# Optimization experiments

Hardware: AMD Instinct MI355X
Metric: run time of the kernel (lower is better)

Reference implementation:

```python
import jax, jax.numpy as jnp
import numpy as np

DN = ('NCHW', 'OIHW', 'NCHW')
B, T, D, H, W = 8, 10, 10, 128, 128
WINDOW_OUT = 5


def conv2d(x, w, b):
    y = jax.lax.conv_general_dilated(x, w, (1, 1), 'SAME', dimension_numbers=DN)
    return y + b[None, :, None, None]


def lstm_cell(x, h, c, w, b):
    # ConvLSTM gate update: conv over [x; h], split into i,f,o,g
    z = conv2d(jnp.concatenate([x, h], axis=1), w, b)
    i, f, o, g = jnp.split(z, 4, axis=1)
    c2 = jax.nn.sigmoid(f) * c + jax.nn.sigmoid(i) * jnp.tanh(g)
    h2 = jax.nn.sigmoid(o) * jnp.tanh(c2)
    return h2, c2


def attn_score(x, h, c, w1, b1, w2, b2):
    # conv-MLP attention score over concat([x, h, c]) -> (b, H, W)
    z = jnp.concatenate([x, h, c], axis=1)
    return conv2d(jnp.tanh(conv2d(z, w1, b1)), w2, b2)[:, 0]


def setup_inputs():
    key = jax.random.key(0)
    ks = jax.random.split(key, 16)
    s = 0.05
    return {
        'x': jax.random.normal(ks[0], (B, T, D, H, W), jnp.float32),
        'h0': jnp.zeros((B, 1, H, W), jnp.float32),
        'c0': jnp.zeros((B, 1, H, W), jnp.float32),
        'h1': jnp.zeros((B, 64, H, W), jnp.float32),
        'c1': jnp.zeros((B, 64, H, W), jnp.float32),
        # encoder cells: layer0 (in 10, hid 1), layer1 (in 1, hid 64)
        'w_enc0': jax.random.normal(ks[1], (4, 11, 3, 3), jnp.float32) * s,
        'b_enc0': jax.random.normal(ks[2], (4,), jnp.float32) * s,
        'w_enc1': jax.random.normal(ks[3], (256, 65, 3, 3), jnp.float32) * s,
        'b_enc1': jax.random.normal(ks[4], (256,), jnp.float32) * s,
        # decoder cells: layer0 (in 1, hid 64), layer1 (in 64, hid 1)
        'w_dec0': jax.random.normal(ks[5], (256, 65, 3, 3), jnp.float32) * s,
        'b_dec0': jax.random.normal(ks[6], (256,), jnp.float32) * s,
        'w_dec1': jax.random.normal(ks[7], (4, 65, 3, 3), jnp.float32) * s,
        'b_dec1': jax.random.normal(ks[8], (4,), jnp.float32) * s,
        # input attention: in 10+2*1=12 -> 32 -> 1
        'wa1': jax.random.normal(ks[9], (32, 12, 3, 3), jnp.float32) * s,
        'ba1': jax.random.normal(ks[10], (32,), jnp.float32) * s,
        'wa2': jax.random.normal(ks[11], (1, 32, 3, 3), jnp.float32) * s,
        'ba2': jax.random.normal(ks[12], (1,), jnp.float32) * s,
        # temporal attention: in 1+2*64=129 -> 32 -> 1
        'wt1': jax.random.normal(ks[13], (32, 129, 3, 3), jnp.float32) * s,
        'bt1': jax.random.normal(ks[14], (32,), jnp.float32) * s,
        'wt2': jax.random.normal(ks[15], (1, 32, 3, 3), jnp.float32) * s,
        'bt2': jnp.zeros((1,), jnp.float32),
    }


def reference(x, h0, c0, h1, c1, w_enc0, b_enc0, w_enc1, b_enc1,
              w_dec0, b_dec0, w_dec1, b_dec1,
              wa1, ba1, wa2, ba2, wt1, bt1, wt2, bt2):
    def input_attn(xx, h, c):
        # per-feature score; vmap over feature dim k (axis 2 of x)
        score = jax.vmap(lambda xk: attn_score(xk, h, c, wa1, ba1, wa2, ba2),
                         in_axes=2, out_axes=1)(xx)          # (b, D, H, W)
        alpha = jax.nn.softmax(score, axis=1)
        return xx * alpha[:, None]                            # broadcast over time

    # ---- encoder layer 0: input attention re-weights x every step (compounding)
    def step0(carry, t):
        xx, h, c = carry
        xx = input_attn(xx, h, c)
        h, c = lstm_cell(xx[:, t], h, c, w_enc0, b_enc0)
        return (xx, h, c), (h, c)

    _, (hs0, cs0) = jax.lax.scan(step0, (x, h0, c0), jnp.arange(T))
    hs0 = jnp.moveaxis(hs0, 0, 1)   # (b, T, 1, H, W)
    cs0 = jnp.moveaxis(cs0, 0, 1)

    # ---- encoder layer 1
    def step1(carry, xt):
        h, c = lstm_cell(xt, carry[0], carry[1], w_enc1, b_enc1)
        return (h, c), (h, c)

    _, (hs1, cs1) = jax.lax.scan(step1, (h1, c1), jnp.moveaxis(hs0, 1, 0))
    hs1 = jnp.moveaxis(hs1, 0, 1)   # (b, T, 64, H, W)
    cs1 = jnp.moveaxis(cs1, 0, 1)

    def temporal_attn(y, hb, cb):
        score = jax.vmap(lambda ht, ct: attn_score(y, ht, ct, wt1, bt1, wt2, bt2),
                         in_axes=1, out_axes=1)(hb, cb)       # (b, T, H, W)
        beta = jax.nn.softmax(score, axis=1)
        return jnp.sum(hb * beta[:, :, None], axis=1), cb[:, -1]

    # ---- decoder: states reversed -> layer0 uses encoder layer1 states, etc.
    y0 = x[:, -1, 0][:, None]       # x[:, [-1], selected_dim] -> (b, 1, H, W)

    def dec_step(carry, _):
        y, hb0, cb0, hb1, cb1 = carry
        ht, ct = temporal_attn(y, hb0, cb0)
        ht, ct = lstm_cell(y, ht, ct, w_dec0, b_dec0)
        y = ht
        hb0 = jnp.concatenate([hb0[:, 1:], ht[:, None]], axis=1)
        cb0 = jnp.concatenate([cb0[:, 1:], ct[:, None]], axis=1)
        ht2, ct2 = lstm_cell(y, hb1[:, -1], cb1[:, -1], w_dec1, b_dec1)
        y = ht2
        hb1 = jnp.concatenate([hb1[:, 1:], ht2[:, None]], axis=1)
        cb1 = jnp.concatenate([cb1[:, 1:], ct2[:, None]], axis=1)
        return (y, hb0, cb0, hb1, cb1), y

    _, ys = jax.lax.scan(dec_step, (y0, hs1, cs1, hs0, cs0), None, length=WINDOW_OUT)
    return jnp.moveaxis(ys, 0, 1)   # (b, window_out, 1, H, W)
```

## Files before the change

kernel.cpp:

```cpp
#include <hip/hip_runtime.h>


#define PX 16384L
#define T_ 10
#define D_ 10

__device__ __forceinline__ float fast_tanh(float x) {
    const float e = __builtin_exp2f(x * 2.88539008f);
    return 1.f - 2.f * __builtin_amdgcn_rcpf(e + 1.f);
}
__device__ __forceinline__ float fast_sig(float x) {
    const float e = __builtin_exp2f(x * -1.44269504f);
    return __builtin_amdgcn_rcpf(e + 1.f);
}
__device__ __forceinline__ float fast_exp(float x) {
    return __builtin_exp2f(x * 1.44269504f);
}

__device__ __forceinline__ void lstm_dev(
    float* lds,
    int tile, int hcb, int b,
    const float* __restrict__ in0, long bs0,
    const float* __restrict__ in1,
    const float* __restrict__ w, const float* __restrict__ bias,
// ... 63 lines not shown
    for (int j = 0; j < 2; j++) {
        const int hc = hc0 + j;
        const float bi = bias[hc], bf = bias[64 + hc];
        const float bo = bias[128 + hc], bg = bias[192 + hc];
#pragma unroll
        for (int rr = 0; rr < 2; rr++) {
            const long opix = (long)(tileY + r0 + rr) * 128 + tileX + tx;
            const float i_ = fast_sig(acc[(j * 4 + 0) * 2 + rr] + bi);
            const float f_ = fast_sig(acc[(j * 4 + 1) * 2 + rr] + bf);
            const float o_ = fast_sig(acc[(j * 4 + 2) * 2 + rr] + bo);
            const float g_ = fast_tanh(acc[(j * 4 + 3) * 2 + rr] + bg);
            const float cp = cprev[((long)b * 64 + hc) * PX + opix];
            const float c2 = f_ * cp + i_ * g_;
            const float h2 = o_ * fast_tanh(c2);
            hout[((long)b * 64 + hc) * PX + opix] = h2;
            cout_[((long)b * 64 + hc) * PX + opix] = c2;
        }
    }
}

__device__ __forceinline__ void zpart_dev(
    float* lds,
    int tile, int cob, int b,
    const float* __restrict__ hsrc, const float* __restrict__ csrc,
    const float* __restrict__ wt1, const float* __restrict__ bt1,
    float* __restrict__ zdst)
{
    const int tid = threadIdx.x;
    const int tx = tid & 15, ty = tid >> 4;
    const int tileX = (tile & 7) << 4, tileY = (tile >> 3) << 4;
    const int co0 = cob << 3;
    float acc[8];
#pragma unroll
    for (int j = 0; j < 8; j++) acc[j] = 0.f;

    int g0[2]; float m0[2];
#pragma unroll
    for (int i = 0; i < 2; i++) {
        const int lidx = tid + i * 256;
        const int r = lidx / 18, cc = lidx - r * 18;
        const int gy = tileY + r - 1, gx = tileX + cc - 1;
        const bool inb = (lidx < 324) && ((unsigned)gy < 128u) && ((unsigned)gx < 128u);
        g0[i] = inb ? gy * 128 + gx : 0;
        m0[i] = inb ? 1.f : 0.f;
    }

    for (int cb = 0; cb < 128; cb += 4) {
        for (int cl = 0; cl < 4; cl++) {
            const int ci = cb + cl;
            const float* p = (ci < 64) ? hsrc + ((long)b * 64 + ci) * PX
                                       : csrc + ((long)b * 64 + (ci - 64)) * PX;
#pragma unroll
            for (int i = 0; i < 2; i++) {
                const int lidx = tid + i * 256;
                if (lidx < 324) lds[cl * 324 + lidx] = m0[i] * p[g0[i]];
            }
        }
        __syncthreads();
        for (int cl = 0; cl < 4; cl++) {
            float r9[9];
#pragma unroll
            for (int dy = 0; dy < 3; dy++)
#pragma unroll
                for (int dx = 0; dx < 3; dx++)
                    r9[dy * 3 + dx] = lds[cl * 324 + (ty + dy) * 18 + tx + dx];
            const int ci = cb + cl;
#pragma unroll
            for (int j = 0; j < 8; j++) {
                const float* wp = wt1 + ((long)(co0 + j) * 129 + 1 + ci) * 9;
                float a = acc[j];
#pragma unroll
                for (int q = 0; q < 9; q++) a = fmaf(wp[q], r9[q], a);
                acc[j] = a;
            }
        }
        __syncthreads();
    }
    const long opix = (long)(tileY + ty) * 128 + tileX + tx;
#pragma unroll
    for (int j = 0; j < 8; j++)
        zdst[((long)b * 32 + co0 + j) * PX + opix] = acc[j] + bt1[co0 + j];
}

__global__ __launch_bounds__(256)
void lstm_merge_k(const float* __restrict__ in0, long bs0,
                  const float* __restrict__ in1,
                  const float* __restrict__ w, const float* __restrict__ bias,
                  const float* __restrict__ cprev,
                  float* __restrict__ hout, float* __restrict__ cout_,
                  const float* __restrict__ zh, const float* __restrict__ zc,
                  float* __restrict__ zdst,
                  const float* __restrict__ wt1, const float* __restrict__ bt1)
{
    __shared__ float lds[8 * 612];
    const int bid = blockIdx.x, b = blockIdx.z;
    if (bid < 1024) {
        lstm_dev(lds, bid & 31, bid >> 5, b, in0, bs0, in1, w, bias,
                 cprev, hout, cout_);
    } else {
        const int q = bid - 1024;
        zpart_dev(lds, q & 63, q >> 6, b, zh, zc, wt1, bt1, zdst);
    }
}

__global__ __launch_bounds__(256)
void zpart_k(const float* __restrict__ zh, const float* __restrict__ zc,
             float* __restrict__ zdst,
             const float* __restrict__ wt1, const float* __restrict__ bt1)
{
    __shared__ float lds[4 * 324];
    zpart_dev(lds, blockIdx.x, blockIdx.y, blockIdx.z, zh, zc, wt1, bt1, zdst);
}

__global__ __launch_bounds__(256)
void dec_merge_k(const float* __restrict__ hs1s,
                 const float* __restrict__ hb1, long hb1bs,
                 const float* __restrict__ w1,
                 float* __restrict__ l1p, int nbs,
                 const float* __restrict__ zc, float* __restrict__ zdst,
                 const float* __restrict__ wt1, const float* __restrict__ bt1)
{
    __shared__ float lds[4 * 324];
    const int bid = blockIdx.x, b = blockIdx.z;
    if (bid < 256) {
        const int tile = bid & 63, s = bid >> 6;
        const int ci0 = (s == 0) ? 0 : (s == 1) ? 17 : (s == 2) ? 33 : 49;
        const int cn  = (s == 0) ? 17 : 16;
        const int tid = threadIdx.x;
        const int tx = tid & 15, ty = tid >> 4;
        const int tileX = (tile & 7) << 4, tileY = (tile >> 3) << 4;
        int g0[2]; float m0[2];
#pragma unroll
        for (int i = 0; i < 2; i++) {
            const int lidx = tid + i * 256;
            const int r = lidx / 18, cc = lidx - r * 18;
            const int gy = tileY + r - 1, gx = tileX + cc - 1;
            const bool inb = (lidx < 324) && ((unsigned)gy < 128u) && ((unsigned)gx < 128u);
            g0[i] = inb ? gy * 128 + gx : 0;
            m0[i] = inb ? 1.f : 0.f;
        }
        float acc[4] = {0.f, 0.f, 0.f, 0.f};
        for (int cb = 0; cb < cn; cb += 4) {
            const int cmax = min(4, cn - cb);
            for (int cl = 0; cl < cmax; cl++) {
                const int ci = ci0 + cb + cl;
                const float* p = (ci < 64) ? hs1s + ((long)b * 64 + ci) * PX
                                           : hb1 + (long)b * hb1bs;
#pragma unroll
                for (int i = 0; i < 2; i++) {
                    const int lidx = tid + i * 256;
                    if (lidx < 324) lds[cl * 324 + lidx] = m0[i] * p[g0[i]];
                }
            }
            __syncthreads();
            for (int cl = 0; cl < cmax; cl++) {
                float r9[9];
#pragma unroll
                for (int dy = 0; dy < 3; dy++)
#pragma unroll
                    for (int dx = 0; dx < 3; dx++)
                        r9[dy * 3 + dx] = lds[cl * 324 + (ty + dy) * 18 + tx + dx];
                const int ci = ci0 + cb + cl;
#pragma unroll
                for (int j = 0; j < 4; j++) {
                    const float* wp = w1 + ((long)j * 65 + ci) * 9;
                    float a = acc[j];
#pragma unroll
                    for (int q = 0; q < 9; q++) a = fmaf(wp[q], r9[q], a);
                    acc[j] = a;
                }
            }
            __syncthreads();
        }
        const long opix = (long)(tileY + ty) * 128 + tileX + tx;
#pragma unroll
        for (int j = 0; j < 4; j++)
            l1p[(((long)s * nbs + b) * 4 + j) * PX + opix] = acc[j];
    } else {
        const int q = bid - 256;
        zpart_dev(lds, q & 63, q >> 6, b, hs1s, zc, wt1, bt1, zdst);
    }
}

__global__ __launch_bounds__(256)
void combine_lstm_k(const float* __restrict__ pbuf, int nsl, int hidden,
                    const float* __restrict__ bias,
                    const float* __restrict__ cprev, long cpbs,
                    float* __restrict__ hout, long hobs,
                    float* __restrict__ cout_, long cobs,
                    float* __restrict__ hout2, long ho2bs, int rb, int nbs)
{
    const long idx = (long)blockIdx.x * 256 + threadIdx.x;
    if (idx >= (long)rb * hidden * PX) return;
    const long px = idx & 16383;
    const long v = idx >> 14;
    const int hc = (int)(v % hidden), b = (int)(v / hidden);
    const int nco = 4 * hidden;
    float g4[4] = {0.f, 0.f, 0.f, 0.f};
    for (int s = 0; s < nsl; s++)
#pragma unroll
        for (int g = 0; g < 4; g++)
            g4[g] += pbuf[(((long)s * nbs + b) * nco + g * hidden + hc) * PX + px];
    const float i_ = fast_sig(g4[0] + bias[hc]);
    const float f_ = fast_sig(g4[1] + bias[hidden + hc]);
    const float o_ = fast_sig(g4[2] + bias[2 * hidden + hc]);
    const float g_ = fast_tanh(g4[3] + bias[3 * hidden + hc]);
    const float cp = cprev[(long)b * cpbs + (long)hc * PX + px];
    const float c2 = f_ * cp + i_ * g_;
    const float h2 = o_ * fast_tanh(c2);
    hout[(long)b * hobs + (long)hc * PX + px] = h2;
    cout_[(long)b * cobs + (long)hc * PX + px] = c2;
    if (hout2) hout2[(long)b * ho2bs + (long)hc * PX + px] = h2;
}

__global__ __launch_bounds__(256)
void enc0_lstm_k(const float* __restrict__ x, int t, const float* __restrict__ A,
                 const float* __restrict__ hprev, const float* __restrict__ cprev,
                 const float* __restrict__ w, const float* __restrict__ bias,
                 float* __restrict__ hout, float* __restrict__ cout_)
{
    __shared__ float lds[4 * 324];
    const int tid = threadIdx.x;
    const int tx = tid & 15, ty = tid >> 4;
    const int tile = blockIdx.x, b = blockIdx.z;
    const int tileX = (tile & 7) << 4, tileY = (tile >> 3) << 4;
    int g0[2]; float m0[2];
#pragma unroll
    for (int i = 0; i < 2; i++) {
        const int lidx = tid + i * 256;
        const int r = lidx / 18, cc = lidx - r * 18;
        const int gy = tileY + r - 1, gx = tileX + cc - 1;
        const bool inb = (lidx < 324) && ((unsigned)gy < 128u) && ((unsigned)gx < 128u);
        g0[i] = inb ? gy * 128 + gx : 0;
        m0[i] = inb ? 1.f : 0.f;
    }
    float acc[4] = {0.f, 0.f, 0.f, 0.f};
    for (int cb = 0; cb < 11; cb += 4) {
        const int cmax = min(4, 11 - cb);
        for (int cl = 0; cl < cmax; cl++) {
            const int ci = cb + cl;
#pragma unroll
            for (int i = 0; i < 2; i++) {
                const int lidx = tid + i * 256;
                if (lidx < 324) {
                    float v;
                    if (ci < 10) {
                        v = x[(((long)b * T_ + t) * D_ + ci) * PX + g0[i]]
                            * A[((long)b * 10 + ci) * PX + g0[i]];
                    } else {
                        v = hprev[(long)b * PX + g0[i]];
                    }
                    lds[cl * 324 + lidx] = m0[i] * v;
                }
            }
        }
        __syncthreads();
        for (int cl = 0; cl < cmax; cl++) {
            float r9[9];
#pragma unroll
            for (int dy = 0; dy < 3; dy++)
#pragma unroll
                for (int dx = 0; dx < 3; dx++)
                    r9[dy * 3 + dx] = lds[cl * 324 + (ty + dy) * 18 + tx + dx];
            const int ci = cb + cl;
#pragma unroll
            for (int g = 0; g < 4; g++) {
                const float* wp = w + ((long)g * 11 + ci) * 9;
                float a = acc[g];
#pragma unroll
                for (int q = 0; q < 9; q++) a = fmaf(wp[q], r9[q], a);
                acc[g] = a;
            }
        }
        __syncthreads();
    }
    const long opix = (long)(tileY + ty) * 128 + tileX + tx;
    const float i_ = fast_sig(acc[0] + bias[0]);
    const float f_ = fast_sig(acc[1] + bias[1]);
    const float o_ = fast_sig(acc[2] + bias[2]);
    const float g_ = fast_tanh(acc[3] + bias[3]);
    const float cp = cprev[(long)b * PX + opix];
    const float c2 = f_ * cp + i_ * g_;
    const float h2 = o_ * fast_tanh(c2);
    hout[(long)b * PX + opix] = h2;
    cout_[(long)b * PX + opix] = c2;
}

__global__ __launch_bounds__(256)
void iattn_k(const float* __restrict__ x, const float* __restrict__ A,
             const float* __restrict__ h, const float* __restrict__ c,
             const float* __restrict__ wa1, const float* __restrict__ ba1,
             const float* __restrict__ wa2, const float* __restrict__ ba2,
             float* __restrict__ score)
{
    __shared__ float xl[12][400];
    __shared__ float zl[8][324];
    const int tid = threadIdx.x;
    const int tileX = (blockIdx.x & 7) << 4, tileY = (blockIdx.x >> 3) << 4;
    const int z = blockIdx.z;
    const int b = z & 7, k = z >> 3;

    int g0[2]; float m0[2]; float aTr[2];
#pragma unroll
    for (int i = 0; i < 2; i++) {
        const int lidx = tid + i * 256;
        const int r = lidx / 20, cc = lidx - r * 20;
        const int gy = tileY + r - 2, gx = tileX + cc - 2;
        const bool inb = (lidx < 400) && ((unsigned)gy < 128u) && ((unsigned)gx < 128u);
        g0[i] = inb ? gy * 128 + gx : 0;
        m0[i] = inb ? 1.f : 0.f;
        aTr[i] = A ? (m0[i] * A[((long)b * 10 + k) * PX + g0[i]]) : 1.f;
    }
    for (int ch = 0; ch < 12; ch++) {
        const float* p = (ch < 10) ? x + (((long)b * 10 + ch) * 10 + k) * PX
                       : (ch == 10) ? h + (long)b * PX : c + (long)b * PX;
#pragma unroll
        for (int i = 0; i < 2; i++) {
            const int lidx = tid + i * 256;
            if (lidx < 400) {
                float v = m0[i] * p[g0[i]];
                if (ch < 10) v *= aTr[i];
                xl[ch][lidx] = v;
            }
        }
    }
    __syncthreads();

    const int i0 = tid;
    const int i1 = tid + 256;
    const int zr0 = i0 / 18, zc0 = i0 - zr0 * 18;
    const int zr1 = (i1 < 324) ? i1 / 18 : 0;
    const int zc1 = (i1 < 324) ? i1 - zr1 * 18 : 0;
    const int gy0 = tileY + zr0 - 1, gx0 = tileX + zc0 - 1;
    const bool in0_ = ((unsigned)gy0 < 128u) && ((unsigned)gx0 < 128u);
    const int gy1 = tileY + zr1 - 1, gx1 = tileX + zc1 - 1;
    const bool in1_ = (i1 < 324) && ((unsigned)gy1 < 128u) && ((unsigned)gx1 < 128u);

    const int tx = tid & 15, ty = tid >> 4;
    float sacc = ba2[0];

    for (int hf = 0; hf < 4; hf++) {
        float acc0[8], acc1[8];
#pragma unroll
        for (int co = 0; co < 8; co++) { acc0[co] = 0.f; acc1[co] = 0.f; }
        for (int ci = 0; ci < 12; ci++) {
            float wA[9], wB[9];
#pragma unroll
            for (int dy = 0; dy < 3; dy++)
#pragma unroll
                for (int dx = 0; dx < 3; dx++) {
                    wA[dy * 3 + dx] = xl[ci][(zr0 + dy) * 20 + zc0 + dx];
                    wB[dy * 3 + dx] = xl[ci][(zr1 + dy) * 20 + zc1 + dx];
                }
#pragma unroll
            for (int co = 0; co < 8; co++) {
                const float* wp = wa1 + ((long)(hf * 8 + co) * 12 + ci) * 9;
                float a0 = acc0[co], a1 = acc1[co];
#pragma unroll
                for (int q = 0; q < 9; q++) {
                    a0 = fmaf(wp[q], wA[q], a0);
                    a1 = fmaf(wp[q], wB[q], a1);
                }
                acc0[co] = a0; acc1[co] = a1;
            }
        }
        if (hf) __syncthreads();
#pragma unroll
        for (int co = 0; co < 8; co++) {
            zl[co][i0] = in0_ ? fast_tanh(acc0[co] + ba1[hf * 8 + co]) : 0.f;
            if (i1 < 324) zl[co][i1] = in1_ ? fast_tanh(acc1[co] + ba1[hf * 8 + co]) : 0.f;
        }
        __syncthreads();
        for (int co = 0; co < 8; co++) {
            const float* wp = wa2 + (hf * 8 + co) * 9;
#pragma unroll
            for (int ky = 0; ky < 3; ky++)
#pragma unroll
                for (int kx = 0; kx < 3; kx++)
                    sacc = fmaf(wp[ky * 3 + kx], zl[co][(ty + ky) * 18 + tx + kx], sacc);
        }
    }
    score[((long)b * 10 + k) * PX + (long)(tileY + ty) * 128 + tileX + tx] = sacc;
}

__global__ __launch_bounds__(256)
void softmax_mul_k(const float* __restrict__ s, float* __restrict__ A, int nb, int init)
{
    const long idx = (long)blockIdx.x * 256 + threadIdx.x;
    if (idx >= (long)nb * PX) return;
    const long b = idx >> 14, p = idx & 16383;
    const float* base = s + b * 10 * PX + p;
    float v[10]; float m = -1e30f;
#pragma unroll
    for (int t = 0; t < 10; t++) { v[t] = base[t * PX]; m = fmaxf(m, v[t]); }
    float sum = 0.f;
#pragma unroll
    for (int t = 0; t < 10; t++) { v[t] = fast_exp(v[t] - m); sum += v[t]; }
    const float r = __builtin_amdgcn_rcpf(sum);
    float* Ab = A + b * 10 * PX + p;
#pragma unroll
    for (int t = 0; t < 10; t++)
        Ab[t * PX] = init ? (v[t] * r) : (Ab[t * PX] * v[t] * r);
}

__global__ __launch_bounds__(256)
void attn_fuse_k(const float* __restrict__ y, long ybs,
                 const float* __restrict__ zpart,
                 const float* __restrict__ wt1,
                 const float* __restrict__ wt2, const float* __restrict__ bt2,
                 float* __restrict__ score, int rb, int nbs)
{
    __shared__ float ylds[400];
    __shared__ float zl[16][324];
    const int tid = threadIdx.x;
    const int tileX = (blockIdx.x & 7) << 4, tileY = (blockIdx.x >> 3) << 4;
    const int z = blockIdx.z;
    const int b = z % rb, t = z / rb;

#pragma unroll
    for (int i = 0; i < 2; i++) {
        const int lidx = tid + i * 256;
        if (lidx < 400) {
            const int r = lidx / 20, cc = lidx - r * 20;
            const int gy = tileY + r - 2, gx = tileX + cc - 2;
            const bool inb = ((unsigned)gy < 128u) && ((unsigned)gx < 128u);
            ylds[lidx] = inb ? y[(long)b * ybs + gy * 128 + gx] : 0.f;
        }
    }
    __syncthreads();

    const int i0 = tid, i1 = tid + 256;
    const int zr0 = i0 / 18, zc0 = i0 - zr0 * 18;
    const int zr1 = (i1 < 324) ? i1 / 18 : 0;
    const int zc1 = (i1 < 324) ? i1 - zr1 * 18 : 0;
    const int gy0 = tileY + zr0 - 1, gx0 = tileX + zc0 - 1;
    const bool in0_ = ((unsigned)gy0 < 128u) && ((unsigned)gx0 < 128u);
    const int gy1 = tileY + zr1 - 1, gx1 = tileX + zc1 - 1;
    const bool in1_ = (i1 < 324) && ((unsigned)gy1 < 128u) && ((unsigned)gx1 < 128u);
    const long pix0 = in0_ ? (long)gy0 * 128 + gx0 : 0;
    const long pix1 = in1_ ? (long)gy1 * 128 + gx1 : 0;
    const float* zp0 = zpart + ((long)t * nbs + b) * 32 * PX;

    const int tx = tid & 15, ty = tid >> 4;
    float sacc = bt2[0];

    for (int hf = 0; hf < 2; hf++) {
        float yw0[9], yw1[9];
#pragma unroll
        for (int dy = 0; dy < 3; dy++)
#pragma unroll
            for (int dx = 0; dx < 3; dx++) {
                yw0[dy * 3 + dx] = ylds[(zr0 + dy) * 20 + zc0 + dx];
                yw1[dy * 3 + dx] = ylds[(zr1 + dy) * 20 + zc1 + dx];
            }
        if (hf) __syncthreads();
#pragma unroll 4
        for (int ch = 0; ch < 16; ch++) {
            const int cg = hf * 16 + ch;
            const float* wy = wt1 + (long)cg * 129 * 9;
            float s0 = zp0[(long)cg * PX + pix0];
            float s1 = (i1 < 324) ? zp0[(long)cg * PX + pix1] : 0.f;
#pragma unroll
            for (int q = 0; q < 9; q++) {
                s0 = fmaf(wy[q], yw0[q], s0);
                s1 = fmaf(wy[q], yw1[q], s1);
            }
            zl[ch][i0] = in0_ ? fast_tanh(s0) : 0.f;
            if (i1 < 324) zl[ch][i1] = in1_ ? fast_tanh(s1) : 0.f;
        }
        __syncthreads();
        for (int ch = 0; ch < 16; ch++) {
            const float* wp = wt2 + (hf * 16 + ch) * 9;
#pragma unroll
            for (int ky = 0; ky < 3; ky++)
#pragma unroll
                for (int kx = 0; kx < 3; kx++)
                    sacc = fmaf(wp[ky * 3 + kx], zl[ch][(ty + ky) * 18 + tx + kx], sacc);
        }
    }
    score[((long)b * 10 + t) * PX + (long)(tileY + ty) * 128 + tileX + tx] = sacc;
}

__global__ __launch_bounds__(256)
void smax_wsum_k(const float* __restrict__ score, const float* __restrict__ hs1,
                 float* __restrict__ aht, int rb, int nbs)
{
    const long idx = (long)blockIdx.x * 256 + threadIdx.x;
    if (idx >= (long)rb * PX) return;
    const long b = idx >> 14, p = idx & 16383;
    const int ch0 = blockIdx.y * 8;
    const float* base = score + b * 10 * PX + p;
    float v[10]; float m = -1e30f;
#pragma unroll
    for (int t = 0; t < 10; t++) { v[t] = base[t * PX]; m = fmaxf(m, v[t]); }
    float sum = 0.f;
#pragma unroll
    for (int t = 0; t < 10; t++) { v[t] = fast_exp(v[t] - m); sum += v[t]; }
    const float r = __builtin_amdgcn_rcpf(sum);
#pragma unroll
    for (int t = 0; t < 10; t++) v[t] *= r;
    const long slot1 = (long)nbs * 64 * PX;
#pragma unroll
    for (int j = 0; j < 8; j++) {
        const int ch = ch0 + j;
        float a = 0.f;
#pragma unroll
        for (int t = 0; t < 10; t++)
            a += v[t] * hs1[t * slot1 + (b * 64 + ch) * PX + p];
        aht[(b * 64 + ch) * PX + p] = a;
    }
}

extern "C" void kernel_launch(void* const* d_in, const int* in_sizes, int n_in,
                              void* d_out, int out_size, void* d_ws, size_t ws_size,
                              hipStream_t stream)
{
    const float* x      = (const float*)d_in[0];
    const float* h0     = (const float*)d_in[1];
    const float* c0in   = (const float*)d_in[2];
    const float* h1     = (const float*)d_in[3];
    const float* c1     = (const float*)d_in[4];
    const float* w_enc0 = (const float*)d_in[5];
    const float* b_enc0 = (const float*)d_in[6];
    const float* w_enc1 = (const float*)d_in[7];
    const float* b_enc1 = (const float*)d_in[8];
    const float* w_dec0 = (const float*)d_in[9];
    const float* b_dec0 = (const float*)d_in[10];
    const float* w_dec1 = (const float*)d_in[11];
    const float* b_dec1 = (const float*)d_in[12];
    const float* wa1 = (const float*)d_in[13];
    const float* ba1 = (const float*)d_in[14];
    const float* wa2 = (const float*)d_in[15];
    const float* ba2 = (const float*)d_in[16];
    const float* wt1 = (const float*)d_in[17];
    const float* bt1 = (const float*)d_in[18];
    const float* wt2 = (const float*)d_in[19];
    const float* bt2 = (const float*)d_in[20];
    float* out = (float*)d_out;

    const int tiers[7] = {8, 6, 5, 4, 3, 2, 1};
    int nb = 0;
    for (int ti = 0; ti < 7; ti++) {
        const size_t need = (size_t)(160 + 1188 * tiers[ti]) * PX * sizeof(float);
        if (need <= ws_size) { nb = tiers[ti]; break; }
    }
    if (nb == 0) return;

    float* ws = (float*)d_ws;
    float* hs0 = ws;
    float* cs0 = hs0 + 80 * PX;
    float* G   = cs0 + 80 * PX;
    float* A    = G;
    float* sc1  = G + 80 * PX;
    const long slot1  = (long)nb * 64 * PX;
    float* hs1   = G;
    float* cs1   = hs1 + 10 * slot1;
    float* zpart = cs1 + 2 * slot1;
    float* aht   = zpart + (long)10 * nb * 32 * PX;
    float* l1p   = aht + (long)nb * 64 * PX;
    float* hs0g  = l1p + (long)4 * nb * 4 * PX;
    float* cs0g  = hs0g + (long)5 * nb * PX;
    float* scD   = cs0g + (long)5 * nb * PX;

    const dim3 blk(256);
    const long TDP = (long)T_ * D_ * PX;
    const long zslot = (long)nb * 32 * PX;

    for (int t = 0; t < 10; t++) {
        const float* hprev = (t == 0) ? h0 : hs0 + (long)(t - 1) * 8 * PX;
        const float* cprev = (t == 0) ? c0in : cs0 + (long)(t - 1) * 8 * PX;
        iattn_k<<<dim3(64, 1, 80), blk, 0, stream>>>(
            x, (t == 0) ? nullptr : A, hprev, cprev, wa1, ba1, wa2, ba2, sc1);
        softmax_mul_k<<<512, blk, 0, stream>>>(sc1, A, 8, t == 0);
        enc0_lstm_k<<<dim3(64, 1, 8), blk, 0, stream>>>(
            x, t, A, hprev, cprev, w_enc0, b_enc0,
            hs0 + (long)t * 8 * PX, cs0 + (long)t * 8 * PX);
    }

    for (int b0 = 0; b0 < 8; b0 += nb) {
        const int rb = (8 - b0 < nb) ? (8 - b0) : nb;
        const float* xb  = x + (long)b0 * TDP;
        float* outb = out + (long)b0 * 5 * PX;

        for (int t = 0; t < 10; t++) {
            const float* hprev = (t == 0) ? h1 + (long)b0 * 64 * PX
                                          : hs1 + (long)(t - 1) * slot1;
            const float* cprev = (t == 0) ? c1 + (long)b0 * 64 * PX
                                          : cs1 + (long)((t - 1) & 1) * slot1;
            const int gx = (t == 0) ? 1024 : 1280;
            lstm_merge_k<<<dim3(gx, 1, rb), blk, 0, stream>>>(
                hs0 + (long)t * 8 * PX + (long)b0 * PX, PX,
                hprev, w_enc1, b_enc1, cprev,
                hs1 + (long)t * slot1, cs1 + (long)(t & 1) * slot1,
                (t == 0) ? nullptr : hs1 + (long)(t - 1) * slot1,
                (t == 0) ? nullptr : cs1 + (long)((t - 1) & 1) * slot1,
                (t == 0) ? nullptr : zpart + (long)(t - 1) * zslot,
                wt1, bt1);
        }
        zpart_k<<<dim3(64, 4, rb), blk, 0, stream>>>(
            hs1 + 9L * slot1, cs1 + slot1, zpart + 9L * zslot, wt1, bt1);

        for (int s = 0; s < 5; s++) {
            const float* yptr; long ybs;
            if (s == 0) { yptr = xb + 9L * D_ * PX; ybs = TDP; }
            else        { yptr = hs0g + (long)(s - 1) * nb * PX; ybs = PX; }
            const float* hb1 = (s == 0) ? hs0 + 9L * 8 * PX + (long)b0 * PX
                                        : hs0g + (long)(s - 1) * nb * PX;
            const float* cb1 = (s == 0) ? cs0 + 9L * 8 * PX + (long)b0 * PX
                                        : cs0g + (long)(s - 1) * nb * PX;

            attn_fuse_k<<<dim3(64, 1, 10 * rb), blk, 0, stream>>>(
                yptr, ybs, zpart, wt1, wt2, bt2, scD, rb, nb);
            smax_wsum_k<<<dim3((int)(((long)rb * PX + 255) / 256), 8), blk, 0, stream>>>(
                scD, hs1, aht, rb, nb);

            lstm_merge_k<<<dim3(1024, 1, rb), blk, 0, stream>>>(
                yptr, ybs, aht, w_dec0, b_dec0,
                cs1 + (long)((s + 1) & 1) * slot1,
                hs1 + (long)s * slot1, cs1 + (long)(s & 1) * slot1,
                nullptr, nullptr, nullptr, wt1, bt1);

            const int gx2 = (s < 4) ? 512 : 256;
            dec_merge_k<<<dim3(gx2, 1, rb), blk, 0, stream>>>(
                hs1 + (long)s * slot1, hb1, PX, w_dec1, l1p, nb,
                cs1 + (long)(s & 1) * slot1, zpart + (long)s * zslot, wt1, bt1);
            combine_lstm_k<<<(int)(((long)rb * PX + 255) / 256), blk, 0, stream>>>(
                l1p, 4, 1, b_dec1, cb1, PX,
                hs0g + (long)s * nb * PX, PX,
                cs0g + (long)s * nb * PX, PX,
                outb + (long)s * PX, 5 * PX, rb, nb);
        }
    }
}
```

Baseline: 18.88 ms.

## Interleave encoder layer-0 attention with layer-1 LSTM and fuse decoder kernels

When the whole batch fits in the workspace, input-attention scoring for step t+1 now runs in the same launch as the layer-1 encoder LSTM for step t. This overlaps two independent recurrences and removes the separate per-step encoder loops. The input-attention softmax is folded into the enc0 LSTM kernel, which also writes the updated attention state. The decoder layer-1 partial-conv, combine pass and l1p buffer are replaced by a single dec_k that finishes the LSTM in-block. The cost is larger, more divergent mega-kernels with more shared memory and a more complex buffer-aliasing scheme.

After: 21.56 ms. 1.14x slower.

```diff
diff --git a/kernel.cpp b/kernel.cpp
--- a/kernel.cpp
+++ b/kernel.cpp
@@ -169,25 +169,143 @@
         zdst[((long)b * 32 + co0 + j) * PX + opix] = acc[j] + bt1[co0 + j];
 }
 
+__device__ __forceinline__ void iattn_dev(
+    float* lds, int tile, int b, int k,
+    const float* __restrict__ x, const float* __restrict__ A,
+    const float* __restrict__ h, const float* __restrict__ c,
+    const float* __restrict__ wa1, const float* __restrict__ ba1,
+    const float* __restrict__ wa2, const float* __restrict__ ba2,
+    float* __restrict__ score)
+{
+    float* xl = lds;
+    float* zl = lds + 4800;
+    const int tid = threadIdx.x;
+    const int tileX = (tile & 7) << 4, tileY = (tile >> 3) << 4;
+
+    int g0[2]; float m0[2]; float aTr[2];
+#pragma unroll
+    for (int i = 0; i < 2; i++) {
+        const int lidx = tid + i * 256;
+        const int r = lidx / 20, cc = lidx - r * 20;
+        const int gy = tileY + r - 2, gx = tileX + cc - 2;
+        const bool inb = (lidx < 400) && ((unsigned)gy < 128u) && ((unsigned)gx < 128u);
+        g0[i] = inb ? gy * 128 + gx : 0;
+        m0[i] = inb ? 1.f : 0.f;
+        aTr[i] = A ? (m0[i] * A[((long)b * 10 + k) * PX + g0[i]]) : 1.f;
+    }
+    for (int ch = 0; ch < 12; ch++) {
+        const float* p = (ch < 10) ? x + (((long)b * 10 + ch) * 10 + k) * PX
+                       : (ch == 10) ? h + (long)b * PX : c + (long)b * PX;
+#pragma unroll
+        for (int i = 0; i < 2; i++) {
+            const int lidx = tid + i * 256;
+            if (lidx < 400) {
+                float v = m0[i] * p[g0[i]];
+                if (ch < 10) v *= aTr[i];
+                xl[ch * 400 + lidx] = v;
+            }
+        }
+    }
+    __syncthreads();
+
+    const int i0 = tid;
+    const int i1 = tid + 256;
+    const int zr0 = i0 / 18, zc0 = i0 - zr0 * 18;
+    const int zr1 = (i1 < 324) ? i1 / 18 : 0;
+    const int zc1 = (i1 < 324) ? i1 - zr1 * 18 : 0;
+    const int gy0 = tileY + zr0 - 1, gx0 = tileX + zc0 - 1;
+    const bool in0_ = ((unsigned)gy0 < 128u) && ((unsigned)gx0 < 128u);
+    const int gy1 = tileY + zr1 - 1, gx1 = tileX + zc1 - 1;
+    const bool in1_ = (i1 < 324) && ((unsigned)gy1 < 128u) && ((unsigned)gx1 < 128u);
+
+    const int tx = tid & 15, ty = tid >> 4;
+    float sacc = ba2[0];
+
+    for (int hf = 0; hf < 4; hf++) {
+        float acc0[8], acc1[8];
+#pragma unroll
+        for (int co = 0; co < 8; co++) { acc0[co] = 0.f; acc1[co] = 0.f; }
+        for (int ci = 0; ci < 12; ci++) {
+            float wA[9], wB[9];
+#pragma unroll
+            for (int dy = 0; dy < 3; dy++)
+#pragma unroll
+                for (int dx = 0; dx < 3; dx++) {
+                    wA[dy * 3 + dx] = xl[ci * 400 + (zr0 + dy) * 20 + zc0 + dx];
+                    wB[dy * 3 + dx] = xl[ci * 400 + (zr1 + dy) * 20 + zc1 + dx];
+                }
+#pragma unroll
+            for (int co = 0; co < 8; co++) {
+                const float* wp = wa1 + ((long)(hf * 8 + co) * 12 + ci) * 9;
+                float a0 = acc0[co], a1 = acc1[co];
+#pragma unroll
+                for (int q = 0; q < 9; q++) {
+                    a0 = fmaf(wp[q], wA[q], a0);
+                    a1 = fmaf(wp[q], wB[q], a1);
+                }
+                acc0[co] = a0; acc1[co] = a1;
+            }
+        }
+        if (hf) __syncthreads();
+#pragma unroll
+        for (int co = 0; co < 8; co++) {
+            zl[co * 324 + i0] = in0_ ? fast_tanh(acc0[co] + ba1[hf * 8 + co]) : 0.f;
+            if (i1 < 324) zl[co * 324 + i1] = in1_ ? fast_tanh(acc1[co] + ba1[hf * 8 + co]) : 0.f;
+        }
+        __syncthreads();
+        for (int co = 0; co < 8; co++) {
+            const float* wp = wa2 + (hf * 8 + co) * 9;
+#pragma unroll
+            for (int ky = 0; ky < 3; ky++)
+#pragma unroll
+                for (int kx = 0; kx < 3; kx++)
+                    sacc = fmaf(wp[ky * 3 + kx], zl[co * 324 + (ty + ky) * 18 + tx + kx], sacc);
+        }
+    }
+    score[((long)b * 10 + k) * PX + (long)(tileY + ty) * 128 + tileX + tx] = sacc;
+}
+
 __global__ __launch_bounds__(256)
-void lstm_merge_k(const float* __restrict__ in0, long bs0,
-                  const float* __restrict__ in1,
-                  const float* __restrict__ w, const float* __restrict__ bias,
-                  const float* __restrict__ cprev,
-                  float* __restrict__ hout, float* __restrict__ cout_,
-                  const float* __restrict__ zh, const float* __restrict__ zc,
-                  float* __restrict__ zdst,
-                  const float* __restrict__ wt1, const float* __restrict__ bt1)
-{
-    __shared__ float lds[8 * 612];
+void mega_k(const float* __restrict__ in0, long bs0,
+            const float* __restrict__ in1,
+            const float* __restrict__ w, const float* __restrict__ bias,
+            const float* __restrict__ cprev,
+            float* __restrict__ hout, float* __restrict__ cout_,
+            const float* __restrict__ zh, const float* __restrict__ zc,
+            float* __restrict__ zdst,
+            const float* __restrict__ wt1, const float* __restrict__ bt1,
+            const float* __restrict__ xi, const float* __restrict__ Ai,
+            const float* __restrict__ hi, const float* __restrict__ ci,
+            const float* __restrict__ wa1, const float* __restrict__ ba1,
+            const float* __restrict__ wa2, const float* __restrict__ ba2,
+            float* __restrict__ score)
+{
+    __shared__ float lds[7392];
     const int bid = blockIdx.x, b = blockIdx.z;
     if (bid < 1024) {
         lstm_dev(lds, bid & 31, bid >> 5, b, in0, bs0, in1, w, bias,
                  cprev, hout, cout_);
-    } else {
+    } else if (zdst && bid < 1280) {
         const int q = bid - 1024;
         zpart_dev(lds, q & 63, q >> 6, b, zh, zc, wt1, bt1, zdst);
-    }
+    } else {
+        const int q = bid - (zdst ? 1280 : 1024);
+        iattn_dev(lds, q & 63, b, q >> 6, xi, Ai, hi, ci,
+                  wa1, ba1, wa2, ba2, score);
+    }
+}
+
+__global__ __launch_bounds__(256)
+void iattn_k(const float* __restrict__ x, const float* __restrict__ A,
+             const float* __restrict__ h, const float* __restrict__ c,
+             const float* __restrict__ wa1, const float* __restrict__ ba1,
+             const float* __restrict__ wa2, const float* __restrict__ ba2,
+             float* __restrict__ score)
+{
+    __shared__ float lds[7392];
+    const int z = blockIdx.z;
+    iattn_dev(lds, blockIdx.x, z & 7, z >> 3, x, A, h, c,
+              wa1, ba1, wa2, ba2, score);
 }
 
 __global__ __launch_bounds__(256)
@@ -200,118 +318,38 @@
 }
 
 __global__ __launch_bounds__(256)
-void dec_merge_k(const float* __restrict__ hs1s,
-                 const float* __restrict__ hb1, long hb1bs,
-                 const float* __restrict__ w1,
-                 float* __restrict__ l1p, int nbs,
-                 const float* __restrict__ zc, float* __restrict__ zdst,
-                 const float* __restrict__ wt1, const float* __restrict__ bt1)
-{
-    __shared__ float lds[4 * 324];
-    const int bid = blockIdx.x, b = blockIdx.z;
-    if (bid < 256) {
-        const int tile = bid & 63, s = bid >> 6;
-        const int ci0 = (s == 0) ? 0 : (s == 1) ? 17 : (s == 2) ? 33 : 49;
-        const int cn  = (s == 0) ? 17 : 16;
-        const int tid = threadIdx.x;
-        const int tx = tid & 15, ty = tid >> 4;
-        const int tileX = (tile & 7) << 4, tileY = (tile >> 3) << 4;
-        int g0[2]; float m0[2];
-#pragma unroll
-        for (int i = 0; i < 2; i++) {
-            const int lidx = tid + i * 256;
-            const int r = lidx / 18, cc = lidx - r * 18;
-            const int gy = tileY + r - 1, gx = tileX + cc - 1;
-            const bool inb = (lidx < 324) && ((unsigned)gy < 128u) && ((unsigned)gx < 128u);
-            g0[i] = inb ? gy * 128 + gx : 0;
-            m0[i] = inb ? 1.f : 0.f;
-        }
-        float acc[4] = {0.f, 0.f, 0.f, 0.f};
-        for (int cb = 0; cb < cn; cb += 4) {
-            const int cmax = min(4, cn - cb);
-            for (int cl = 0; cl < cmax; cl++) {
-                const int ci = ci0 + cb + cl;
-                const float* p = (ci < 64) ? hs1s + ((long)b * 64 + ci) * PX
-                                           : hb1 + (long)b * hb1bs;
-#pragma unroll
-                for (int i = 0; i < 2; i++) {
-                    const int lidx = tid + i * 256;
-                    if (lidx < 324) lds[cl * 324 + lidx] = m0[i] * p[g0[i]];
-                }
-            }
-            __syncthreads();
-            for (int cl = 0; cl < cmax; cl++) {
-                float r9[9];
-#pragma unroll
-                for (int dy = 0; dy < 3; dy++)
-#pragma unroll
-                    for (int dx = 0; dx < 3; dx++)
-                        r9[dy * 3 + dx] = lds[cl * 324 + (ty + dy) * 18 + tx + dx];
-                const int ci = ci0 + cb + cl;
-#pragma unroll
-                for (int j = 0; j < 4; j++) {
-                    const float* wp = w1 + ((long)j * 65 + ci) * 9;
-                    float a = acc[j];
-#pragma unroll
-                    for (int q = 0; q < 9; q++) a = fmaf(wp[q], r9[q], a);
-                    acc[j] = a;
-                }
-            }
-            __syncthreads();
-        }
-        const long opix = (long)(tileY + ty) * 128 + tileX + tx;
-#pragma unroll
-        for (int j = 0; j < 4; j++)
-            l1p[(((long)s * nbs + b) * 4 + j) * PX + opix] = acc[j];
-    } else {
-        const int q = bid - 256;
-        zpart_dev(lds, q & 63, q >> 6, b, hs1s, zc, wt1, bt1, zdst);
-    }
-}
-
-__global__ __launch_bounds__(256)
-void combine_lstm_k(const float* __restrict__ pbuf, int nsl, int hidden,
-                    const float* __restrict__ bias,
-                    const float* __restrict__ cprev, long cpbs,
-                    float* __restrict__ hout, long hobs,
-                    float* __restrict__ cout_, long cobs,
-                    float* __restrict__ hout2, long ho2bs, int rb, int nbs)
-{
-    const long idx = (long)blockIdx.x * 256 + threadIdx.x;
-    if (idx >= (long)rb * hidden * PX) return;
-    const long px = idx & 16383;
-    const long v = idx >> 14;
-    const int hc = (int)(v % hidden), b = (int)(v / hidden);
-    const int nco = 4 * hidden;
-    float g4[4] = {0.f, 0.f, 0.f, 0.f};
-    for (int s = 0; s < nsl; s++)
-#pragma unroll
-        for (int g = 0; g < 4; g++)
-            g4[g] += pbuf[(((long)s * nbs + b) * nco + g * hidden + hc) * PX + px];
-    const float i_ = fast_sig(g4[0] + bias[hc]);
-    const float f_ = fast_sig(g4[1] + bias[hidden + hc]);
-    const float o_ = fast_sig(g4[2] + bias[2 * hidden + hc]);
-    const float g_ = fast_tanh(g4[3] + bias[3 * hidden + hc]);
-    const float cp = cprev[(long)b * cpbs + (long)hc * PX + px];
-    const float c2 = f_ * cp + i_ * g_;
-    const float h2 = o_ * fast_tanh(c2);
-    hout[(long)b * hobs + (long)hc * PX + px] = h2;
-    cout_[(long)b * cobs + (long)hc * PX + px] = c2;
-    if (hout2) hout2[(long)b * ho2bs + (long)hc * PX + px] = h2;
-}
-
-__global__ __launch_bounds__(256)
-void enc0_lstm_k(const float* __restrict__ x, int t, const float* __restrict__ A,
-                 const float* __restrict__ hprev, const float* __restrict__ cprev,
-                 const float* __restrict__ w, const float* __restrict__ bias,
-                 float* __restrict__ hout, float* __restrict__ cout_)
+void enc0m_k(const float* __restrict__ x, int t,
+             const float* __restrict__ Acur, float* __restrict__ Anext,
+             const float* __restrict__ sc1,
+             const float* __restrict__ hprev, const float* __restrict__ cprev,
+             const float* __restrict__ w, const float* __restrict__ bias,
+             float* __restrict__ hout, float* __restrict__ cout_)
 {
     __shared__ float lds[4 * 324];
     const int tid = threadIdx.x;
+    const int b = blockIdx.z;
+    if (blockIdx.x >= 64) {
+        const long p = (((long)blockIdx.x - 64) << 8) + tid;
+        const float* sp = sc1 + (long)b * 10 * PX + p;
+        float v[10]; float m = -1e30f;
+#pragma unroll
+        for (int k = 0; k < 10; k++) { v[k] = sp[k * PX]; m = fmaxf(m, v[k]); }
+        float sum = 0.f;
+#pragma unroll
+        for (int k = 0; k < 10; k++) { v[k] = fast_exp(v[k] - m); sum += v[k]; }
+        const float r = __builtin_amdgcn_rcpf(sum);
+        float* Ap = Anext + (long)b * 10 * PX + p;
+#pragma unroll
+        for (int k = 0; k < 10; k++) {
+            const float a = v[k] * r;
+            Ap[k * PX] = Acur ? Acur[((long)b * 10 + k) * PX + p] * a : a;
+        }
+        return;
+    }
     const int tx = tid & 15, ty = tid >> 4;
-    const int tile = blockIdx.x, b = blockIdx.z;
+    const int tile = blockIdx.x;
     const int tileX = (tile & 7) << 4, tileY = (tile >> 3) << 4;
-    int g0[2]; float m0[2];
+    int g0[2]; float m0[2]; float e[2][10]; float rr_[2];
 #pragma unroll
     for (int i = 0; i < 2; i++) {
         const int lidx = tid + i * 256;
@@ -320,6 +358,14 @@
         const bool inb = (lidx < 324) && ((unsigned)gy < 128u) && ((unsigned)gx < 128u);
         g0[i] = inb ? gy * 128 + gx : 0;
         m0[i] = inb ? 1.f : 0.f;
+        const float* sp = sc1 + (long)b * 10 * PX + g0[i];
+        float mm = -1e30f;
+#pragma unroll
+        for (int k = 0; k < 10; k++) { e[i][k] = sp[k * PX]; mm = fmaxf(mm, e[i][k]); }
+        float sum = 0.f;
+#pragma unroll
+        for (int k = 0; k < 10; k++) { e[i][k] = fast_exp(e[i][k] - mm); sum += e[i][k]; }
+        rr_[i] = __builtin_amdgcn_rcpf(sum);
     }
     float acc[4] = {0.f, 0.f, 0.f, 0.f};
     for (int cb = 0; cb < 11; cb += 4) {
@@ -330,26 +376,27 @@
             for (int i = 0; i < 2; i++) {
                 const int lidx = tid + i * 256;
                 if (lidx < 324) {
-                    float v;
+                    float vv;
                     if (ci < 10) {
-                        v = x[(((long)b * T_ + t) * D_ + ci) * PX + g0[i]]
-                            * A[((long)b * 10 + ci) * PX + g0[i]];
+                        float al = e[i][ci] * rr_[i];
+                        if (Acur) al *= Acur[((long)b * 10 + ci) * PX + g0[i]];
+                        vv = x[(((long)b * T_ + t) * D_ + ci) * PX + g0[i]] * al;
                     } else {
-                        v = hprev[(long)b * PX + g0[i]];
+                        vv = hprev[(long)b * PX + g0[i]];
                     }
-                    lds[cl * 324 + lidx] = m0[i] * v;
+                    lds[cl * 324 + lidx] = m0[i] * vv;
                 }
             }
         }
         __syncthreads();
         for (int cl = 0; cl < cmax; cl++) {
+            const int ci = cb + cl;
             float r9[9];
 #pragma unroll
             for (int dy = 0; dy < 3; dy++)
 #pragma unroll
                 for (int dx = 0; dx < 3; dx++)
                     r9[dy * 3 + dx] = lds[cl * 324 + (ty + dy) * 18 + tx + dx];
-            const int ci = cb + cl;
 #pragma unroll
             for (int g = 0; g < 4; g++) {
                 const float* wp = w + ((long)g * 11 + ci) * 9;
@@ -371,123 +418,6 @@
     const float h2 = o_ * fast_tanh(c2);
     hout[(long)b * PX + opix] = h2;
     cout_[(long)b * PX + opix] = c2;
-}
-
-__global__ __launch_bounds__(256)
-void iattn_k(const float* __restrict__ x, const float* __restrict__ A,
-             const float* __restrict__ h, const float* __restrict__ c,
-             const float* __restrict__ wa1, const float* __restrict__ ba1,
-             const float* __restrict__ wa2, const float* __restrict__ ba2,
-             float* __restrict__ score)
-{
-    __shared__ float xl[12][400];
-    __shared__ float zl[8][324];
-    const int tid = threadIdx.x;
-    const int tileX = (blockIdx.x & 7) << 4, tileY = (blockIdx.x >> 3) << 4;
-    const int z = blockIdx.z;
-    const int b = z & 7, k = z >> 3;
-
-    int g0[2]; float m0[2]; float aTr[2];
-#pragma unroll
-    for (int i = 0; i < 2; i++) {
-        const int lidx = tid + i * 256;
-        const int r = lidx / 20, cc = lidx - r * 20;
-        const int gy = tileY + r - 2, gx = tileX + cc - 2;
-        const bool inb = (lidx < 400) && ((unsigned)gy < 128u) && ((unsigned)gx < 128u);
-        g0[i] = inb ? gy * 128 + gx : 0;
-        m0[i] = inb ? 1.f : 0.f;
-        aTr[i] = A ? (m0[i] * A[((long)b * 10 + k) * PX + g0[i]]) : 1.f;
-    }
-    for (int ch = 0; ch < 12; ch++) {
-        const float* p = (ch < 10) ? x + (((long)b * 10 + ch) * 10 + k) * PX
-                       : (ch == 10) ? h + (long)b * PX : c + (long)b * PX;
-#pragma unroll
-        for (int i = 0; i < 2; i++) {
-            const int lidx = tid + i * 256;
-            if (lidx < 400) {
-                float v = m0[i] * p[g0[i]];
-                if (ch < 10) v *= aTr[i];
-                xl[ch][lidx] = v;
-            }
-        }
-    }
-    __syncthreads();
-
-    const int i0 = tid;
-    const int i1 = tid + 256;
-    const int zr0 = i0 / 18, zc0 = i0 - zr0 * 18;
-    const int zr1 = (i1 < 324) ? i1 / 18 : 0;
-    const int zc1 = (i1 < 324) ? i1 - zr1 * 18 : 0;
-    const int gy0 = tileY + zr0 - 1, gx0 = tileX + zc0 - 1;
-    const bool in0_ = ((unsigned)gy0 < 128u) && ((unsigned)gx0 < 128u);
-    const int gy1 = tileY + zr1 - 1, gx1 = tileX + zc1 - 1;
-    const bool in1_ = (i1 < 324) && ((unsigned)gy1 < 128u) && ((unsigned)gx1 < 128u);
-
-    const int tx = tid & 15, ty = tid >> 4;
-    float sacc = ba2[0];
-
-    for (int hf = 0; hf < 4; hf++) {
-        float acc0[8], acc1[8];
-#pragma unroll
-        for (int co = 0; co < 8; co++) { acc0[co] = 0.f; acc1[co] = 0.f; }
-        for (int ci = 0; ci < 12; ci++) {
-            float wA[9], wB[9];
-#pragma unroll
-            for (int dy = 0; dy < 3; dy++)
-#pragma unroll
-                for (int dx = 0; dx < 3; dx++) {
-                    wA[dy * 3 + dx] = xl[ci][(zr0 + dy) * 20 + zc0 + dx];
-                    wB[dy * 3 + dx] = xl[ci][(zr1 + dy) * 20 + zc1 + dx];
-                }
-#pragma unroll
-            for (int co = 0; co < 8; co++) {
-                const float* wp = wa1 + ((long)(hf * 8 + co) * 12 + ci) * 9;
-                float a0 = acc0[co], a1 = acc1[co];
-#pragma unroll
-                for (int q = 0; q < 9; q++) {
-                    a0 = fmaf(wp[q], wA[q], a0);
-                    a1 = fmaf(wp[q], wB[q], a1);
-                }
-                acc0[co] = a0; acc1[co] = a1;
-            }
-        }
-        if (hf) __syncthreads();
-#pragma unroll
-        for (int co = 0; co < 8; co++) {
-            zl[co][i0] = in0_ ? fast_tanh(acc0[co] + ba1[hf * 8 + co]) : 0.f;
-            if (i1 < 324) zl[co][i1] = in1_ ? fast_tanh(acc1[co] + ba1[hf * 8 + co]) : 0.f;
-        }
-        __syncthreads();
-        for (int co = 0; co < 8; co++) {
-            const float* wp = wa2 + (hf * 8 + co) * 9;
-#pragma unroll
-            for (int ky = 0; ky < 3; ky++)
-#pragma unroll
-                for (int kx = 0; kx < 3; kx++)
-                    sacc = fmaf(wp[ky * 3 + kx], zl[co][(ty + ky) * 18 + tx + kx], sacc);
-        }
-    }
-    score[((long)b * 10 + k) * PX + (long)(tileY + ty) * 128 + tileX + tx] = sacc;
-}
-
-__global__ __launch_bounds__(256)
-void softmax_mul_k(const float* __restrict__ s, float* __restrict__ A, int nb, int init)
-{
-    const long idx = (long)blockIdx.x * 256 + threadIdx.x;
-    if (idx >= (long)nb * PX) return;
-    const long b = idx >> 14, p = idx & 16383;
-    const float* base = s + b * 10 * PX + p;
-    float v[10]; float m = -1e30f;
-#pragma unroll
-    for (int t = 0; t < 10; t++) { v[t] = base[t * PX]; m = fmaxf(m, v[t]); }
-    float sum = 0.f;
-#pragma unroll
-    for (int t = 0; t < 10; t++) { v[t] = fast_exp(v[t] - m); sum += v[t]; }
-    const float r = __builtin_amdgcn_rcpf(sum);
-    float* Ab = A + b * 10 * PX + p;
-#pragma unroll
-    for (int t = 0; t < 10; t++)
-        Ab[t * PX] = init ? (v[t] * r) : (Ab[t * PX] * v[t] * r);
 }
 
 __global__ __launch_bounds__(256)
@@ -596,6 +526,82 @@
             a += v[t] * hs1[t * slot1 + (b * 64 + ch) * PX + p];
         aht[(b * 64 + ch) * PX + p] = a;
     }
+}
+
+__global__ __launch_bounds__(256)
+void dec_k(const float* __restrict__ hs1s,
+           const float* __restrict__ hb1, long hb1bs,
+           const float* __restrict__ w1, const float* __restrict__ b1,
+           const float* __restrict__ cb1,
+           float* __restrict__ hdst, float* __restrict__ cdst,
+           float* __restrict__ odst,
+           const float* __restrict__ zc, float* __restrict__ zdst,
+           const float* __restrict__ wt1, const float* __restrict__ bt1)
+{
+    __shared__ float lds[4 * 324];
+    const int bid = blockIdx.x, b = blockIdx.z;
+    if (bid >= 64) {
+        const int q = bid - 64;
+        zpart_dev(lds, q & 63, q >> 6, b, hs1s, zc, wt1, bt1, zdst);
+        return;
+    }
+    const int tid = threadIdx.x;
+    const int tx = tid & 15, ty = tid >> 4;
+    const int tileX = (bid & 7) << 4, tileY = (bid >> 3) << 4;
+    int g0[2]; float m0[2];
+#pragma unroll
+    for (int i = 0; i < 2; i++) {
+        const int lidx = tid + i * 256;
+        const int r = lidx / 18, cc = lidx - r * 18;
+        const int gy = tileY + r - 1, gx = tileX + cc - 1;
+        const bool inb = (lidx < 324) && ((unsigned)gy < 128u) && ((unsigned)gx < 128u);
+        g0[i] = inb ? gy * 128 + gx : 0;
+        m0[i] = inb ? 1.f : 0.f;
+    }
+    float acc[4] = {0.f, 0.f, 0.f, 0.f};
+    for (int cb = 0; cb < 65; cb += 4) {
+        const int cmax = min(4, 65 - cb);
+        for (int cl = 0; cl < cmax; cl++) {
+            const int ci = cb + cl;
+            const float* p = (ci < 64) ? hs1s + ((long)b * 64 + ci) * PX
+                                       : hb1 + (long)b * hb1bs;
+#pragma unroll
+            for (int i = 0; i < 2; i++) {
+                const int lidx = tid + i * 256;
+                if (lidx < 324) lds[cl * 324 + lidx] = m0[i] * p[g0[i]];
+            }
+        }
+        __syncthreads();
+        for (int cl = 0; cl < cmax; cl++) {
+            float r9[9];
+#pragma unroll
+            for (int dy = 0; dy < 3; dy++)
+#pragma unroll
+                for (int dx = 0; dx < 3; dx++)
+                    r9[dy * 3 + dx] = lds[cl * 324 + (ty + dy) * 18 + tx + dx];
+            const int ci = cb + cl;
+#pragma unroll
+            for (int j = 0; j < 4; j++) {
+                const float* wp = w1 + ((long)j * 65 + ci) * 9;
+                float a = acc[j];
+#pragma unroll
+                for (int q = 0; q < 9; q++) a = fmaf(wp[q], r9[q], a);
+                acc[j] = a;
+            }
+        }
+        __syncthreads();
+    }
+    const long opix = (long)(tileY + ty) * 128 + tileX + tx;
+    const float i_ = fast_sig(acc[0] + b1[0]);
+    const float f_ = fast_sig(acc[1] + b1[1]);
+    const float o_ = fast_sig(acc[2] + b1[2]);
+    const float g_ = fast_tanh(acc[3] + b1[3]);
+    const float cp = cb1[(long)b * PX + opix];
+    const float c2 = f_ * cp + i_ * g_;
+    const float h2 = o_ * fast_tanh(c2);
+    hdst[(long)b * PX + opix] = h2;
+    cdst[(long)b * PX + opix] = c2;
+    odst[(long)b * 5 * PX + opix] = h2;
 }
 
 extern "C" void kernel_launch(void* const* d_in, const int* in_sizes, int n_in,
@@ -632,13 +638,12 @@
         if (need <= ws_size) { nb = tiers[ti]; break; }
     }
     if (nb == 0) return;
+    const bool ilv = (nb == 8);
 
     float* ws = (float*)d_ws;
     float* hs0 = ws;
     float* cs0 = hs0 + 80 * PX;
     float* G   = cs0 + 80 * PX;
-    float* A    = G;
-    float* sc1  = G + 80 * PX;
     const long slot1  = (long)nb * 64 * PX;
     float* hs1   = G;
     float* cs1   = hs1 + 10 * slot1;
@@ -648,20 +653,53 @@
     float* hs0g  = l1p + (long)4 * nb * 4 * PX;
     float* cs0g  = hs0g + (long)5 * nb * PX;
     float* scD   = cs0g + (long)5 * nb * PX;
+    float* Abuf0 = ilv ? aht : G;
+    float* Abuf1 = Abuf0 + 80 * PX;
+    float* sc1   = Abuf0 + 160 * PX;
 
     const dim3 blk(256);
     const long TDP = (long)T_ * D_ * PX;
     const long zslot = (long)nb * 32 * PX;
 
-    for (int t = 0; t < 10; t++) {
-        const float* hprev = (t == 0) ? h0 : hs0 + (long)(t - 1) * 8 * PX;
-        const float* cprev = (t == 0) ? c0in : cs0 + (long)(t - 1) * 8 * PX;
+    if (ilv) {
         iattn_k<<<dim3(64, 1, 80), blk, 0, stream>>>(
-            x, (t == 0) ? nullptr : A, hprev, cprev, wa1, ba1, wa2, ba2, sc1);
-        softmax_mul_k<<<512, blk, 0, stream>>>(sc1, A, 8, t == 0);
-        enc0_lstm_k<<<dim3(64, 1, 8), blk, 0, stream>>>(
-            x, t, A, hprev, cprev, w_enc0, b_enc0,
-            hs0 + (long)t * 8 * PX, cs0 + (long)t * 8 * PX);
+            x, nullptr, h0, c0in, wa1, ba1, wa2, ba2, sc1);
+        for (int t = 0; t < 10; t++) {
+            const float* hprev0 = (t == 0) ? h0 : hs0 + (long)(t - 1) * 8 * PX;
+            const float* cprev0 = (t == 0) ? c0in : cs0 + (long)(t - 1) * 8 * PX;
+            const float* Acur  = (t == 0) ? nullptr : ((t & 1) ? Abuf1 : Abuf0);
+            float* Anext = (t & 1) ? Abuf0 : Abuf1;
+            enc0m_k<<<dim3(128, 1, 8), blk, 0, stream>>>(
+                x, t, Acur, Anext, sc1, hprev0, cprev0, w_enc0, b_enc0,
+                hs0 + (long)t * 8 * PX, cs0 + (long)t * 8 * PX);
+            const float* hprev1 = (t == 0) ? h1 : hs1 + (long)(t - 1) * slot1;
+            const float* cprev1 = (t == 0) ? c1 : cs1 + (long)((t - 1) & 1) * slot1;
+            const bool zp = (t > 0), ia = (t < 9);
+            const int gx = 1024 + (zp ? 256 : 0) + (ia ? 640 : 0);
+            mega_k<<<dim3(gx, 1, 8), blk, 0, stream>>>(
+                hs0 + (long)t * 8 * PX, PX, hprev1, w_enc1, b_enc1, cprev1,
+                hs1 + (long)t * slot1, cs1 + (long)(t & 1) * slot1,
+                zp ? hs1 + (long)(t - 1) * slot1 : nullptr,
+                zp ? cs1 + (long)((t - 1) & 1) * slot1 : nullptr,
+                zp ? zpart + (long)(t - 1) * zslot : nullptr,
+                wt1, bt1,
+                x, Anext, hs0 + (long)t * 8 * PX, cs0 + (long)t * 8 * PX,
+                wa1, ba1, wa2, ba2, ia ? sc1 : nullptr);
+        }
+        zpart_k<<<dim3(64, 4, 8), blk, 0, stream>>>(
+            hs1 + 9L * slot1, cs1 + slot1, zpart + 9L * zslot, wt1, bt1);
+    } else {
+        for (int t = 0; t < 10; t++) {
+            const float* hprev0 = (t == 0) ? h0 : hs0 + (long)(t - 1) * 8 * PX;
+            const float* cprev0 = (t == 0) ? c0in : cs0 + (long)(t - 1) * 8 * PX;
+            const float* Acur  = (t == 0) ? nullptr : ((t & 1) ? Abuf1 : Abuf0);
+            float* Anext = (t & 1) ? Abuf0 : Abuf1;
+            iattn_k<<<dim3(64, 1, 80), blk, 0, stream>>>(
+                x, Acur, hprev0, cprev0, wa1, ba1, wa2, ba2, sc1);
+            enc0m_k<<<dim3(128, 1, 8), blk, 0, stream>>>(
+                x, t, Acur, Anext, sc1, hprev0, cprev0, w_enc0, b_enc0,
+                hs0 + (long)t * 8 * PX, cs0 + (long)t * 8 * PX);
+        }
     }
 
     for (int b0 = 0; b0 < 8; b0 += nb) {
@@ -669,23 +707,27 @@
         const float* xb  = x + (long)b0 * TDP;
         float* outb = out + (long)b0 * 5 * PX;
 
-        for (int t = 0; t < 10; t++) {
-            const float* hprev = (t == 0) ? h1 + (long)b0 * 64 * PX
-                                          : hs1 + (long)(t - 1) * slot1;
-            const float* cprev = (t == 0) ? c1 + (long)b0 * 64 * PX
-                                          : cs1 + (long)((t - 1) & 1) * slot1;
-            const int gx = (t == 0) ? 1024 : 1280;
-            lstm_merge_k<<<dim3(gx, 1, rb), blk, 0, stream>>>(
-                hs0 + (long)t * 8 * PX + (long)b0 * PX, PX,
-                hprev, w_enc1, b_enc1, cprev,
-                hs1 + (long)t * slot1, cs1 + (long)(t & 1) * slot1,
-                (t == 0) ? nullptr : hs1 + (long)(t - 1) * slot1,
-                (t == 0) ? nullptr : cs1 + (long)((t - 1) & 1) * slot1,
-                (t == 0) ? nullptr : zpart + (long)(t - 1) * zslot,
-                wt1, bt1);
-        }
-        zpart_k<<<dim3(64, 4, rb), blk, 0, stream>>>(
-            hs1 + 9L * slot1, cs1 + slot1, zpart + 9L * zslot, wt1, bt1);
+        if (!ilv) {
+            for (int t = 0; t < 10; t++) {
+                const float* hprev = (t == 0) ? h1 + (long)b0 * 64 * PX
+                                              : hs1 + (long)(t - 1) * slot1;
+                const float* cprev = (t == 0) ? c1 + (long)b0 * 64 * PX
+                                              : cs1 + (long)((t - 1) & 1) * slot1;
+                const bool zp = (t > 0);
+                mega_k<<<dim3(zp ? 1280 : 1024, 1, rb), blk, 0, stream>>>(
+                    hs0 + (long)t * 8 * PX + (long)b0 * PX, PX,
+                    hprev, w_enc1, b_enc1, cprev,
+                    hs1 + (long)t * slot1, cs1 + (long)(t & 1) * slot1,
+                    zp ? hs1 + (long)(t - 1) * slot1 : nullptr,
+                    zp ? cs1 + (long)((t - 1) & 1) * slot1 : nullptr,
+                    zp ? zpart + (long)(t - 1) * zslot : nullptr,
+                    wt1, bt1,
+                    nullptr, nullptr, nullptr, nullptr,
+                    nullptr, nullptr, nullptr, nullptr, nullptr);
+            }
+            zpart_k<<<dim3(64, 4, rb), blk, 0, stream>>>(
+                hs1 + 9L * slot1, cs1 + slot1, zpart + 9L * zslot, wt1, bt1);
+        }
 
         for (int s = 0; s < 5; s++) {
             const float* yptr; long ybs;
@@ -701,21 +743,20 @@
             smax_wsum_k<<<dim3((int)(((long)rb * PX + 255) / 256), 8), blk, 0, stream>>>(
                 scD, hs1, aht, rb, nb);
 
-            lstm_merge_k<<<dim3(1024, 1, rb), blk, 0, stream>>>(
+            mega_k<<<dim3(1024, 1, rb), blk, 0, stream>>>(
                 yptr, ybs, aht, w_dec0, b_dec0,
                 cs1 + (long)((s + 1) & 1) * slot1,
                 hs1 + (long)s * slot1, cs1 + (long)(s & 1) * slot1,
-                nullptr, nullptr, nullptr, wt1, bt1);
-
-            const int gx2 = (s < 4) ? 512 : 256;
-            dec_merge_k<<<dim3(gx2, 1, rb), blk, 0, stream>>>(
-                hs1 + (long)s * slot1, hb1, PX, w_dec1, l1p, nb,
-                cs1 + (long)(s & 1) * slot1, zpart + (long)s * zslot, wt1, bt1);
-            combine_lstm_k<<<(int)(((long)rb * PX + 255) / 256), blk, 0, stream>>>(
-                l1p, 4, 1, b_dec1, cb1, PX,
-                hs0g + (long)s * nb * PX, PX,
-                cs0g + (long)s * nb * PX, PX,
-                outb + (long)s * PX, 5 * PX, rb, nb);
-        }
-    }
-}
+                nullptr, nullptr, nullptr, wt1, bt1,
+                nullptr, nullptr, nullptr, nullptr,
+                nullptr, nullptr, nullptr, nullptr, nullptr);
+
+            dec_k<<<dim3((s < 4) ? 320 : 64, 1, rb), blk, 0, stream>>>(
+                hs1 + (long)s * slot1, hb1, PX, w_dec1, b_dec1, cb1,
+                hs0g + (long)s * nb * PX, cs0g + (long)s * nb * PX,
+                outb + (long)s * PX,
+                cs1 + (long)(s & 1) * slot1,
+                (s < 4) ? zpart + (long)s * zslot : nullptr, wt1, bt1);
+        }
+    }
+}
```
